# Performance work log

Measured on AMD Instinct MI355X. Metric: run time of the kernel, lower is better.

## Reference

```python
import jax, jax.numpy as jnp
import numpy as np
import math

B, S, E, H, FF = 2, 2048, 1024, 16, 4096
HD = E // H
EPS = 1e-6


def layer_norm(x, gamma, beta):
    mu = jnp.mean(x, axis=-1, keepdims=True)
    var = jnp.mean(jnp.square(x - mu), axis=-1, keepdims=True)
    return (x - mu) * jax.lax.rsqrt(var + EPS) * gamma + beta


def setup_inputs() -> dict:
    key = jax.random.key(0)
    ks = jax.random.split(key, 8)
    x_embeds = jax.random.normal(ks[0], (B, S, E), dtype=jnp.float32)
    # causal mask: True means masked (j > i), broadcastable over batch/heads
    mask = jnp.triu(jnp.ones((S, S), dtype=bool), k=1)[None, None]
    sc = 1.0 / math.sqrt(E)
    w_kqv = jax.random.normal(ks[1], (3 * E, E), dtype=jnp.float32) * sc
    w_o = jax.random.normal(ks[2], (E, E), dtype=jnp.float32) * sc
    w_up = jax.random.normal(ks[3], (FF, E), dtype=jnp.float32) * sc
    b_up = jnp.zeros((FF,), dtype=jnp.float32)
    w_down = jax.random.normal(ks[4], (E, FF), dtype=jnp.float32) / math.sqrt(FF)
    b_down = jnp.zeros((E,), dtype=jnp.float32)
    g1 = jnp.ones((E,), dtype=jnp.float32)
    b1 = jnp.zeros((E,), dtype=jnp.float32)
    g2 = jnp.ones((E,), dtype=jnp.float32)
    b2 = jnp.zeros((E,), dtype=jnp.float32)
    return {"x_embeds": x_embeds, "mask": mask, "w_kqv": w_kqv, "w_o": w_o,
            "w_up": w_up, "b_up": b_up, "w_down": w_down, "b_down": b_down,
            "g1": g1, "b1": b1, "g2": g2, "b2": b2}


def reference(x_embeds, mask, w_kqv, w_o, w_up, b_up, w_down, b_down, g1, b1, g2, b2):
    b, s = x_embeds.shape[0], x_embeds.shape[1]
    # --- attention ---
    kqv = x_embeds @ w_kqv.T                      # [B,S,3E]
    kqv = kqv.reshape(b, s, 3, H, HD).transpose(0, 3, 2, 1, 4)  # [B,H,3,S,HD]
    xk, xq, xv = kqv[:, :, 0], kqv[:, :, 1], kqv[:, :, 2]
    attn = jnp.einsum('bhqd,bhkd->bhqk', xq, xk) / math.sqrt(HD)
    attn = jnp.where(mask, -jnp.inf, attn)
    attn = jax.nn.softmax(attn, axis=-1)
    out = jnp.einsum('bhqk,bhkd->bhqd', attn, xv)  # [B,H,S,HD]
    out = out.transpose(0, 2, 1, 3).reshape(b, s, E)
    out = out @ w_o.T
    x = layer_norm(out + x_embeds, g1, b1)
    # --- ffnn ---
    h = jax.nn.relu(x @ w_up.T + b_up)
    h = h @ w_down.T + b_down
    return layer_norm(h + x, g2, b2)
```

## Files before the change

### kernel.cpp

```cpp
#include <hip/hip_runtime.h>
#include <stdint.h>

#define B_ 2
#define S_ 2048
#define E_ 1024
#define H_ 16
#define HD_ 64
#define FF_ 4096
#define M_ 4096

typedef short bf16x8 __attribute__((ext_vector_type(8)));
typedef float f32x4  __attribute__((ext_vector_type(4)));
typedef short shortx4 __attribute__((ext_vector_type(4)));

#define MFMA16(a,b,c) __builtin_amdgcn_mfma_f32_16x16x32_bf16(a,b,c,0,0,0)

__device__ __forceinline__ short f2bf(float f) {
  uint32_t u = __builtin_bit_cast(uint32_t, f);
  u += 0x7fffu + ((u >> 16) & 1u);
  return (short)(u >> 16);
}
__device__ __forceinline__ float bf2f(short b) {
  uint32_t u = ((uint32_t)(uint16_t)b) << 16;
  return __builtin_bit_cast(float, u);
}

template<int CTRL>
__device__ __forceinline__ float dpp_ror(float x) {
  return __builtin_bit_cast(float,
    __builtin_amdgcn_update_dpp(0, __builtin_bit_cast(int, x), CTRL, 0xF, 0xF, true));
}
__device__ __forceinline__ float dpp_max16(float v) {
  v = fmaxf(v, dpp_ror<0x128>(v));
  v = fmaxf(v, dpp_ror<0x124>(v));
  v = fmaxf(v, dpp_ror<0x122>(v));
  v = fmaxf(v, dpp_ror<0x121>(v));
  return v;
}
__device__ __forceinline__ float dpp_sum16(float v) {
  v += dpp_ror<0x128>(v);
  v += dpp_ror<0x124>(v);
  v += dpp_ror<0x122>(v);
  v += dpp_ror<0x121>(v);
  return v;
}

#define GLDS16(g, l) __builtin_amdgcn_global_load_lds( \
    (const __attribute__((address_space(1))) unsigned int*)(g), \
    (__attribute__((address_space(3))) unsigned int*)(l), 16, 0, 0)

__global__ void cast_all(const float* __restrict__ x, const float* __restrict__ wkqv,
                         const float* __restrict__ wo, const float* __restrict__ wup,
                         const float* __restrict__ wdown,
                         short* __restrict__ xb, short* __restrict__ wkqvb,
                         short* __restrict__ wob, short* __restrict__ wupb,
                         short* __restrict__ wdownb) {
  const int stride = gridDim.x * blockDim.x;
  for (int i = blockIdx.x * blockDim.x + threadIdx.x; i < 4194304; i += stride) {
    const int e = i << 2;
    const float* src; short* dst; int off;
    if (e < 4194304)       { src = x;     dst = xb;     off = e; }
    else if (e < 7340032)  { src = wkqv;  dst = wkqvb;  off = e - 4194304; }
    else if (e < 8388608)  { src = wo;    dst = wob;    off = e - 7340032; }
    else if (e < 12582912) { src = wup;   dst = wupb;   off = e - 8388608; }
    else                   { src = wdown; dst = wdownb; off = e - 12582912; }
    float4 v = *(const float4*)(src + off);
    shortx4 o;
    o.x = f2bf(v.x); o.y = f2bf(v.y); o.z = f2bf(v.z); o.w = f2bf(v.w);
    *(shortx4*)(dst + off) = o;
  }
}

template<int SK, int EPI, typename OutT>
__global__ __launch_bounds__(256) void gemm_bt(
    const short* __restrict__ A, const short* __restrict__ Bw,
    OutT* __restrict__ C0, OutT* __restrict__ C1, const float* __restrict__ bias,
    int M, int N, int K)
{
  __shared__ short Al[128 * 32];
  __shared__ short Bl[128 * 32];
  const int tid  = threadIdx.x;
  const int w    = tid >> 6, lane = tid & 63;
  const int ntiles = N >> 7;
  const int nwg = gridDim.x;
  const int bid = blockIdx.x;
  const int swz = (bid & 7) * (nwg >> 3) + (bid >> 3);
  const int tn = swz % ntiles, tm = swz / ntiles;
  const int m0 = tm << 7, n0 = tn << 7;
  const int wr = (w >> 1) << 6, wc = (w & 1) << 6;
  const int lr = lane & 15, lk = (lane >> 4) << 3;
  const int ra = lane >> 2, colA = (lane & 3) << 3;

  const int kper = K / SK;
  const int kbeg = (SK > 1) ? (int)blockIdx.y * kper : 0;
  const int kend = kbeg + kper;
  OutT* __restrict__ C = (SK > 1 && blockIdx.y) ? C1 : C0;

  f32x4 acc[4][4] = {};

  for (int k0 = kbeg; k0 < kend; k0 += 32) {
    __syncthreads();
    #pragma unroll
    for (int i = 0; i < 2; ++i) {
      const int ch = w + (i << 2);
      GLDS16(A  + (size_t)(m0 + ch * 16 + ra) * K + k0 + colA, &Al[ch * 512]);
      GLDS16(Bw + (size_t)(n0 + ch * 16 + ra) * K + k0 + colA, &Bl[ch * 512]);
    }
    __syncthreads();
    bf16x8 af[4], bfr[4];
    #pragma unroll
    for (int i = 0; i < 4; ++i)
      af[i] = *(const bf16x8*)&Al[(wr + i * 16 + lr) * 32 + lk];
    #pragma unroll
    for (int j = 0; j < 4; ++j)
      bfr[j] = *(const bf16x8*)&Bl[(wc + j * 16 + lr) * 32 + lk];
    #pragma unroll
    for (int i = 0; i < 4; ++i)
      #pragma unroll
      for (int j = 0; j < 4; ++j)
        acc[i][j] = MFMA16(af[i], bfr[j], acc[i][j]);
  }

  const int lg = lane >> 4;
  #pragma unroll
  for (int j = 0; j < 4; ++j) {
    const int col = n0 + wc + j * 16 + lr;
    float bv = 0.f;
    if constexpr (SK == 1 && EPI != 0) bv = bias[col];
    #pragma unroll
    for (int i = 0; i < 4; ++i) {
      #pragma unroll
      for (int r = 0; r < 4; ++r) {
        const int row = m0 + wr + i * 16 + lg * 4 + r;
        float v = acc[i][j][r] + bv;
        if constexpr (SK == 1 && EPI == 1) v = fmaxf(v, 0.f);
        if constexpr (sizeof(OutT) == 2) C[(size_t)row * N + col] = f2bf(v);
        else                             C[(size_t)row * N + col] = v;
      }
    }
  }
}

__global__ __launch_bounds__(256) void attn_kernel(
    const short* __restrict__ kqv, short* __restrict__ out)
{
  __shared__ short Kt[64][72];
  __shared__ short Vt[64][72];
  __shared__ short Pl[4][16][72];

  const int tid = threadIdx.x, w = tid >> 6, lane = tid & 63;
  const int p = blockIdx.x;
  const int bh = blockIdx.y;
  const int b = bh >> 4, h = bh & 15;
  const int q0lo = p << 6, q0hi = (31 - p) << 6;
  const int nkb = 32 - p;
  const int lr = lane & 15, lg = lane >> 4;

  const size_t rowlo = (size_t)(b * S_ + q0lo + w * 16 + lr) * 3072 + 1024 + h * 64;
  const size_t rowhi = (size_t)(b * S_ + q0hi + w * 16 + lr) * 3072 + 1024 + h * 64;
  bf16x8 qlo[2], qhi[2];
  qlo[0] = *(const bf16x8*)&kqv[rowlo + lg * 8];
  qlo[1] = *(const bf16x8*)&kqv[rowlo + 32 + lg * 8];
  qhi[0] = *(const bf16x8*)&kqv[rowhi + lg * 8];
  qhi[1] = *(const bf16x8*)&kqv[rowhi + 32 + lg * 8];
  #pragma unroll
  for (int ks = 0; ks < 2; ++ks)
    #pragma unroll
    for (int e = 0; e < 8; ++e) {
      qlo[ks][e] = f2bf(bf2f(qlo[ks][e]) * 0.125f);
      qhi[ks][e] = f2bf(bf2f(qhi[ks][e]) * 0.125f);
    }

  f32x4 aclo[4] = {}, achi[4] = {};
  float mlo[4], llo[4], mhi[4], lhi[4];
  #pragma unroll
  for (int r = 0; r < 4; ++r) { mlo[r] = mhi[r] = -1e30f; llo[r] = lhi[r] = 0.f; }

  const int skk = tid >> 3;
  const int sc  = (tid & 7) << 3;
  const int vws = (tid & 7) << 3;

  for (int kbi = 0; kbi < nkb; ++kbi) {
    const int kb = kbi << 6;
    #pragma unroll
    for (int i = 0; i < 2; ++i) {
      const int krow = skk + i * 32;
      const size_t gb = (size_t)(b * S_ + kb + krow) * 3072 + h * 64 + sc;
      *(bf16x8*)&Kt[krow][sc] = *(const bf16x8*)&kqv[gb];
      bf16x8 vv = *(const bf16x8*)&kqv[gb + 2048];
      const int kc = krow ^ vws;
      #pragma unroll
      for (int e = 0; e < 8; ++e) Vt[sc + e][kc] = vv[e];
    }
    __syncthreads();

    auto process = [&](const bf16x8 (&qf)[2], f32x4 (&acc)[4],
                       float (&m_run)[4], float (&l_run)[4], int q0) {
      f32x4 sacc[4] = {};
      __builtin_amdgcn_s_setprio(1);
      #pragma unroll
      for (int jt = 0; jt < 4; ++jt) {
        #pragma unroll
        for (int ks = 0; ks < 2; ++ks) {
          bf16x8 kf = *(const bf16x8*)&Kt[jt * 16 + lr][ks * 32 + lg * 8];
          sacc[jt] = MFMA16(qf[ks], kf, sacc[jt]);
        }
      }
      __builtin_amdgcn_s_setprio(0);
      float rmax[4];
      #pragma unroll
      for (int r = 0; r < 4; ++r) rmax[r] = -1e30f;
      #pragma unroll
      for (int jt = 0; jt < 4; ++jt) {
        const int kpos = kb + jt * 16 + lr;
        #pragma unroll
        for (int r = 0; r < 4; ++r) {
          const int qrow = q0 + w * 16 + lg * 4 + r;
          float v = sacc[jt][r];
          v = (kpos <= qrow) ? v : -1e30f;
          sacc[jt][r] = v;
          rmax[r] = fmaxf(rmax[r], v);
        }
      }
      #pragma unroll
      for (int r = 0; r < 4; ++r) rmax[r] = dpp_max16(rmax[r]);
      float alpha[4], rsum[4];
      #pragma unroll
      for (int r = 0; r < 4; ++r) {
        float mn = fmaxf(m_run[r], rmax[r]);
        alpha[r] = __expf(m_run[r] - mn);
        m_run[r] = mn;
        rsum[r] = 0.f;
      }
      #pragma unroll
      for (int jt = 0; jt < 4; ++jt)
        #pragma unroll
        for (int r = 0; r < 4; ++r) {
          float pv = __expf(sacc[jt][r] - m_run[r]);
          sacc[jt][r] = pv;
          rsum[r] += pv;
        }
      #pragma unroll
      for (int r = 0; r < 4; ++r) rsum[r] = dpp_sum16(rsum[r]);
      #pragma unroll
      for (int r = 0; r < 4; ++r) l_run[r] = l_run[r] * alpha[r] + rsum[r];
      #pragma unroll
      for (int dt = 0; dt < 4; ++dt)
        #pragma unroll
        for (int r = 0; r < 4; ++r) acc[dt][r] *= alpha[r];
      #pragma unroll
      for (int jt = 0; jt < 4; ++jt)
        #pragma unroll
        for (int r = 0; r < 4; ++r)
          Pl[w][lg * 4 + r][jt * 16 + lr] = f2bf(sacc[jt][r]);
      bf16x8 pa[2];
      pa[0] = *(const bf16x8*)&Pl[w][lr][lg * 8];
      pa[1] = *(const bf16x8*)&Pl[w][lr][32 + lg * 8];
      __builtin_amdgcn_s_setprio(1);
      #pragma unroll
      for (int dt = 0; dt < 4; ++dt) {
        const int vswz = (2 * dt + (lr >> 3)) << 3;
        #pragma unroll
        for (int ks = 0; ks < 2; ++ks) {
          bf16x8 vb = *(const bf16x8*)&Vt[dt * 16 + lr][(ks * 32 + lg * 8) ^ vswz];
          acc[dt] = MFMA16(pa[ks], vb, acc[dt]);
        }
      }
      __builtin_amdgcn_s_setprio(0);
    };

    process(qhi, achi, mhi, lhi, q0hi);
    if (kb <= q0lo + w * 16 + 15) process(qlo, aclo, mlo, llo, q0lo);
    __syncthreads();
  }

  #pragma unroll
  for (int dt = 0; dt < 4; ++dt) {
    #pragma unroll
    for (int r = 0; r < 4; ++r) {
      const int d = h * 64 + dt * 16 + lr;
      const int qlo_row = q0lo + w * 16 + lg * 4 + r;
      const int qhi_row = q0hi + w * 16 + lg * 4 + r;
      out[(size_t)(b * S_ + qlo_row) * E_ + d] = f2bf(aclo[dt][r] / llo[r]);
      out[(size_t)(b * S_ + qhi_row) * E_ + d] = f2bf(achi[dt][r] / lhi[r]);
    }
  }
}

template<int FINAL>
__global__ __launch_bounds__(256) void ln_kernel(
    const float* __restrict__ y0, const float* __restrict__ y1,
    const float* __restrict__ bias, const void* __restrict__ res,
    const float* __restrict__ gam, const float* __restrict__ bet,
    void* __restrict__ outp)
{
  const int row = blockIdx.x, tid = threadIdx.x, lane = tid & 63, w = tid >> 6;
  float4 a = ((const float4*)(y0 + (size_t)row * E_))[tid];
  float4 c = ((const float4*)(y1 + (size_t)row * E_))[tid];
  float r[4] = {a.x + c.x, a.y + c.y, a.z + c.z, a.w + c.w};
  if constexpr (FINAL) {
    float4 bi = ((const float4*)bias)[tid];
    shortx4 rb = ((const shortx4*)((const short*)res + (size_t)row * E_))[tid];
    r[0] += bi.x + bf2f(rb.x); r[1] += bi.y + bf2f(rb.y);
    r[2] += bi.z + bf2f(rb.z); r[3] += bi.w + bf2f(rb.w);
  } else {
    float4 rv = ((const float4*)((const float*)res + (size_t)row * E_))[tid];
    r[0] += rv.x; r[1] += rv.y; r[2] += rv.z; r[3] += rv.w;
  }
  float s  = r[0] + r[1] + r[2] + r[3];
  float ss = r[0]*r[0] + r[1]*r[1] + r[2]*r[2] + r[3]*r[3];
  #pragma unroll
  for (int m = 32; m >= 1; m >>= 1) { s += __shfl_xor(s, m); ss += __shfl_xor(ss, m); }
  __shared__ float red[8];
  if (lane == 0) { red[w] = s; red[4 + w] = ss; }
  __syncthreads();
  s  = red[0] + red[1] + red[2] + red[3];
  ss = red[4] + red[5] + red[6] + red[7];
  const float mu  = s * (1.f / E_);
  const float var = ss * (1.f / E_) - mu * mu;
  const float rs  = rsqrtf(var + 1e-6f);
  float4 gv = ((const float4*)gam)[tid];
  float4 bv = ((const float4*)bet)[tid];
  float o0 = (r[0] - mu) * rs * gv.x + bv.x;
  float o1 = (r[1] - mu) * rs * gv.y + bv.y;
  float o2 = (r[2] - mu) * rs * gv.z + bv.z;
  float o3 = (r[3] - mu) * rs * gv.w + bv.w;
  if constexpr (FINAL) {
    float4 o; o.x = o0; o.y = o1; o.z = o2; o.w = o3;
    ((float4*)((float*)outp + (size_t)row * E_))[tid] = o;
  } else {
    shortx4 o; o.x = f2bf(o0); o.y = f2bf(o1); o.z = f2bf(o2); o.w = f2bf(o3);
    ((shortx4*)((short*)outp + (size_t)row * E_))[tid] = o;
  }
}

extern "C" void kernel_launch(void* const* d_in, const int* in_sizes, int n_in,
                              void* d_out, int out_size, void* d_ws, size_t ws_size,
                              hipStream_t stream) {
  const float* x      = (const float*)d_in[0];
  const float* w_kqv  = (const float*)d_in[2];
  const float* w_o    = (const float*)d_in[3];
  const float* w_up   = (const float*)d_in[4];
  const float* b_up   = (const float*)d_in[5];
  const float* w_down = (const float*)d_in[6];
  const float* b_down = (const float*)d_in[7];
  const float* g1     = (const float*)d_in[8];
  const float* b1     = (const float*)d_in[9];
  const float* g2     = (const float*)d_in[10];
  const float* b2     = (const float*)d_in[11];
  float* out = (float*)d_out;

  char* ws = (char*)d_ws;
  short* xb     = (short*)(ws);
  short* wkqvb  = (short*)(ws + ((size_t)8  << 20));
  short* wob    = (short*)(ws + ((size_t)14 << 20));
  short* wupb   = (short*)(ws + ((size_t)16 << 20));
  short* wdownb = (short*)(ws + ((size_t)24 << 20));
  short* kqv    = (short*)(ws + ((size_t)32 << 20));
  float* proj0  = (float*)(ws + ((size_t)32 << 20));
  float* proj1  = (float*)(ws + ((size_t)48 << 20));
  short* hbuf   = (short*)(ws + ((size_t)32 << 20));
  short* attno  = (short*)(ws + ((size_t)64 << 20));
  short* xln    = (short*)(ws + ((size_t)72 << 20));
  float* down0  = (float*)(ws);
  float* down1  = (float*)(ws + ((size_t)80 << 20));

  cast_all<<<2048, 256, 0, stream>>>(x, w_kqv, w_o, w_up, w_down,
                                     xb, wkqvb, wob, wupb, wdownb);

  gemm_bt<1, 0, short><<<24 * 32, 256, 0, stream>>>(xb, wkqvb, kqv, nullptr, nullptr, M_, 3 * E_, E_);
  attn_kernel<<<dim3(16, B_ * H_), 256, 0, stream>>>(kqv, attno);
  gemm_bt<2, 0, float><<<dim3(256, 2), 256, 0, stream>>>(attno, wob, proj0, proj1, nullptr, M_, E_, E_);
  ln_kernel<0><<<M_, 256, 0, stream>>>(proj0, proj1, nullptr, x, g1, b1, xln);
  gemm_bt<1, 1, short><<<32 * 32, 256, 0, stream>>>(xln, wupb, hbuf, nullptr, b_up, M_, FF_, E_);
  gemm_bt<2, 0, float><<<dim3(256, 2), 256, 0, stream>>>(hbuf, wdownb, down0, down1, nullptr, M_, E_, FF_);
  ln_kernel<1><<<M_, 256, 0, stream>>>(down0, down1, b_down, xln, g2, b2, out);
}
```

Before: 277.3 us.

## Streamline online softmax: skip masking on full tiles, lazy rescale, exp2, packed bf16 cvt

In the attention inner loop, the causal mask is now applied only on diagonal tiles and skipped for fully visible tiles. The running max is updated only when some row's new max exceeds the stored one by more than a threshold (lazy rescaling), which skips the accumulator rescale most of the time. Exponentials use the hardware v_exp_f32 on log2e-scaled inputs via FMA. P is converted to bf16 with the packed v_cvt_pk_bf16_f32 instruction instead of manual rounding. The lazy rescale relies on exp values bounded by 2^(8*log2e), which stays safe in fp32 but could change bf16 P precision slightly.

```diff
diff --git a/kernel.cpp b/kernel.cpp
--- a/kernel.cpp
+++ b/kernel.cpp
@@ -8,6 +8,7 @@
 #define HD_ 64
 #define FF_ 4096
 #define M_ 4096
+#define LOG2E_ 1.44269504f
 
 typedef short bf16x8 __attribute__((ext_vector_type(8)));
 typedef float f32x4  __attribute__((ext_vector_type(4)));
@@ -23,6 +24,11 @@
 __device__ __forceinline__ float bf2f(short b) {
   uint32_t u = ((uint32_t)(uint16_t)b) << 16;
   return __builtin_bit_cast(float, u);
+}
+__device__ __forceinline__ float exp2_hw(float x) {
+  float r;
+  asm("v_exp_f32 %0, %1" : "=v"(r) : "v"(x));
+  return r;
 }
 
 template<int CTRL>
@@ -207,52 +213,66 @@
         }
       }
       __builtin_amdgcn_s_setprio(0);
+      const bool full = (kb + 63 <= q0 + w * 16);
       float rmax[4];
-      #pragma unroll
-      for (int r = 0; r < 4; ++r) rmax[r] = -1e30f;
-      #pragma unroll
-      for (int jt = 0; jt < 4; ++jt) {
-        const int kpos = kb + jt * 16 + lr;
+      if (full) {
+        #pragma unroll
+        for (int r = 0; r < 4; ++r)
+          rmax[r] = fmaxf(fmaxf(sacc[0][r], sacc[1][r]), fmaxf(sacc[2][r], sacc[3][r]));
+      } else {
+        #pragma unroll
+        for (int r = 0; r < 4; ++r) rmax[r] = -1e30f;
+        #pragma unroll
+        for (int jt = 0; jt < 4; ++jt) {
+          const int kpos = kb + jt * 16 + lr;
+          #pragma unroll
+          for (int r = 0; r < 4; ++r) {
+            const int qrow = q0 + w * 16 + lg * 4 + r;
+            float v = (kpos <= qrow) ? sacc[jt][r] : -1e30f;
+            sacc[jt][r] = v;
+            rmax[r] = fmaxf(rmax[r], v);
+          }
+        }
+      }
+      #pragma unroll
+      for (int r = 0; r < 4; ++r) rmax[r] = dpp_max16(rmax[r]);
+      int need = 0;
+      #pragma unroll
+      for (int r = 0; r < 4; ++r) need |= (rmax[r] > m_run[r] + 8.f) ? 1 : 0;
+      if (__any(need)) {
         #pragma unroll
         for (int r = 0; r < 4; ++r) {
-          const int qrow = q0 + w * 16 + lg * 4 + r;
-          float v = sacc[jt][r];
-          v = (kpos <= qrow) ? v : -1e30f;
-          sacc[jt][r] = v;
-          rmax[r] = fmaxf(rmax[r], v);
-        }
-      }
-      #pragma unroll
-      for (int r = 0; r < 4; ++r) rmax[r] = dpp_max16(rmax[r]);
-      float alpha[4], rsum[4];
-      #pragma unroll
-      for (int r = 0; r < 4; ++r) {
-        float mn = fmaxf(m_run[r], rmax[r]);
-        alpha[r] = __expf(m_run[r] - mn);
-        m_run[r] = mn;
-        rsum[r] = 0.f;
-      }
+          const float mn = fmaxf(m_run[r], rmax[r]);
+          const float al = exp2_hw((m_run[r] - mn) * LOG2E_);
+          m_run[r] = mn;
+          l_run[r] *= al;
+          #pragma unroll
+          for (int dt = 0; dt < 4; ++dt) acc[dt][r] *= al;
+        }
+      }
+      float m2[4], rsum[4];
+      #pragma unroll
+      for (int r = 0; r < 4; ++r) { m2[r] = m_run[r] * LOG2E_; rsum[r] = 0.f; }
       #pragma unroll
       for (int jt = 0; jt < 4; ++jt)
         #pragma unroll
         for (int r = 0; r < 4; ++r) {
-          float pv = __expf(sacc[jt][r] - m_run[r]);
+          const float pv = exp2_hw(__builtin_fmaf(sacc[jt][r], LOG2E_, -m2[r]));
           sacc[jt][r] = pv;
           rsum[r] += pv;
         }
       #pragma unroll
-      for (int r = 0; r < 4; ++r) rsum[r] = dpp_sum16(rsum[r]);
-      #pragma unroll
-      for (int r = 0; r < 4; ++r) l_run[r] = l_run[r] * alpha[r] + rsum[r];
-      #pragma unroll
-      for (int dt = 0; dt < 4; ++dt)
-        #pragma unroll
-        for (int r = 0; r < 4; ++r) acc[dt][r] *= alpha[r];
-      #pragma unroll
-      for (int jt = 0; jt < 4; ++jt)
-        #pragma unroll
-        for (int r = 0; r < 4; ++r)
-          Pl[w][lg * 4 + r][jt * 16 + lr] = f2bf(sacc[jt][r]);
+      for (int r = 0; r < 4; ++r) { rsum[r] = dpp_sum16(rsum[r]); l_run[r] += rsum[r]; }
+      #pragma unroll
+      for (int jt = 0; jt < 4; ++jt) {
+        uint32_t w01, w23;
+        asm("v_cvt_pk_bf16_f32 %0, %1, %2" : "=v"(w01) : "v"(sacc[jt][0]), "v"(sacc[jt][1]));
+        asm("v_cvt_pk_bf16_f32 %0, %1, %2" : "=v"(w23) : "v"(sacc[jt][2]), "v"(sacc[jt][3]));
+        Pl[w][lg * 4 + 0][jt * 16 + lr] = (short)(w01 & 0xffffu);
+        Pl[w][lg * 4 + 1][jt * 16 + lr] = (short)(w01 >> 16);
+        Pl[w][lg * 4 + 2][jt * 16 + lr] = (short)(w23 & 0xffffu);
+        Pl[w][lg * 4 + 3][jt * 16 + lr] = (short)(w23 >> 16);
+      }
       bf16x8 pa[2];
       pa[0] = *(const bf16x8*)&Pl[w][lr][lg * 8];
       pa[1] = *(const bf16x8*)&Pl[w][lr][32 + lg * 8];
```

After: 277.2 us. No clear change (-0.0%).
